# Optimization experiments

Measured on AMD Instinct MI355X. Metric: run time of the kernel, lower is better.

Reference implementation:

```python
import jax, jax.numpy as jnp
import numpy as np

WS = 4           # window_size
NUM_HEADS = 4
LN_EPS = 1e-5


def setup_inputs() -> dict:
    key = jax.random.key(0)
    ks = jax.random.split(key, 8)
    d = 256
    s = 0.02
    return {
        "feature": jax.random.normal(ks[0], (8, d, 127, 127), dtype=jnp.float32),
        "ln_w": jnp.ones((d,), jnp.float32),
        "ln_b": jnp.zeros((d,), jnp.float32),
        "in_w": jax.random.normal(ks[1], (3 * d, d), jnp.float32) * s,
        "in_b": jnp.zeros((3 * d,), jnp.float32),
        "out_w": jax.random.normal(ks[2], (d, d), jnp.float32) * s,
        "out_b": jnp.zeros((d,), jnp.float32),
        "proj_w": jax.random.normal(ks[3], (d, d), jnp.float32) * s,
        "proj_b": jnp.zeros((d,), jnp.float32),
    }


def reference(feature, ln_w, ln_b, in_w, in_b, out_w, out_b, proj_w, proj_b):
    B, C, H, W = feature.shape
    ws = WS
    pad_h = (-H) % ws
    pad_w = (-W) % ws
    x = jnp.pad(feature, ((0, 0), (0, 0), (0, pad_h), (0, pad_w)))
    Hp, Wp = H + pad_h, W + pad_w
    nh, nw = Hp // ws, Wp // ws
    # NCHW -> NHWC -> windows [B*nh*nw, ws*ws, C]
    x = x.transpose(0, 2, 3, 1)
    win = (x.reshape(B, nh, ws, nw, ws, C)
            .transpose(0, 1, 3, 2, 4, 5)
            .reshape(-1, ws * ws, C))
    # LayerNorm (ddof=0, matches torch)
    mu = win.mean(-1, keepdims=True)
    var = win.var(-1, keepdims=True)
    xn = (win - mu) / jnp.sqrt(var + LN_EPS) * ln_w + ln_b
    # fused QKV projection, then split heads
    qkv = xn @ in_w.T + in_b
    q, k, v = jnp.split(qkv, 3, axis=-1)
    hd = C // NUM_HEADS
    def heads(t):
        return t.reshape(t.shape[0], t.shape[1], NUM_HEADS, hd).transpose(0, 2, 1, 3)
    q, k, v = heads(q), heads(k), heads(v)
    scores = jnp.einsum('bhqd,bhkd->bhqk', q, k) / np.float32(np.sqrt(hd))
    a = jax.nn.softmax(scores, axis=-1)
    o = jnp.einsum('bhqk,bhkd->bhqd', a, v)
    o = o.transpose(0, 2, 1, 3).reshape(-1, ws * ws, C)
    o = o @ out_w.T + out_b
    # residual + Linear + exact GELU
    y = win + jax.nn.gelu(o @ proj_w.T + proj_b, approximate=False)
    # windows -> NHWC, crop padding, -> NCHW
    y = (y.reshape(B, nh, nw, ws, ws, C)
          .transpose(0, 1, 3, 2, 4, 5)
          .reshape(B, Hp, Wp, C))
    return y[:, :H, :W, :].transpose(0, 3, 1, 2)
```

## Files before the change

kernel.cpp:

```cpp
#include <hip/hip_runtime.h>

typedef _Float16 f16;
typedef __attribute__((ext_vector_type(4))) _Float16 half4;
typedef __attribute__((ext_vector_type(8))) _Float16 half8;
typedef __attribute__((ext_vector_type(4))) float f32x4;
typedef unsigned short u16;

#define MFMA32(a,b,c) __builtin_amdgcn_mfma_f32_16x16x32_f16(a,b,c,0,0,0)
#define MFMA16(a,b,c) __builtin_amdgcn_mfma_f32_16x16x16f16(a,b,c,0,0,0)

#define W_IN0   0
#define W_OUT0  196608
#define W_PROJ0 262144
#define X0      327680
#define QK0     33882112ull
#define VT0     100990976ull

__device__ __forceinline__ float gelu_f(float x) {
    float z = x * 0.70710678118f;
    float az = fabsf(z);
    float t = 1.f / (1.f + 0.3275911f * az);
    float e = __expf(-z * z);
    float poly = ((((1.061405429f * t - 1.453152027f) * t + 1.421413741f) * t
                   - 0.284496736f) * t + 0.254829592f) * t;
    float er = 1.f - poly * e;
    er = copysignf(er, z);
    return 0.5f * x * (1.f + er);
}

__global__ void k0_cast(const float* __restrict__ iw, const float* __restrict__ ow,
                        const float* __restrict__ pw, f16* __restrict__ W) {
    int i = blockIdx.x * 256 + threadIdx.x;
    if (i < 196608) W[W_IN0 + i] = (f16)iw[i];
    if (i < 16384) {
        const int s = i & 8191;
        const float* src = (i < 8192) ? ow : pw;
        f16* dst = W + ((i < 8192) ? W_OUT0 : W_PROJ0);
        const int g  = s & 3;
        const int r  = (s >> 2) & 31;
        const int kc = (s >> 7) & 7;
        const int ch = s >> 10;
        const int R = ch * 32 + r;
        const int c0 = kc * 32 + g * 4;
        f32x4 v0 = *(const f32x4*)(src + R * 256 + c0);
        f32x4 v1 = *(const f32x4*)(src + R * 256 + c0 + 16);
        half8 o;
#pragma unroll
        for (int j = 0; j < 4; ++j) { o[j] = (f16)v0[j]; o[j + 4] = (f16)v1[j]; }
        const int sg = g ^ ((r >> 1) & 3);
        *(half8*)(dst + ch * 8192 + kc * 1024 + r * 32 + sg * 8) = o;
    }
}

__global__ __launch_bounds__(256, 2)
void k1_pack(const float* __restrict__ feat, const float* __restrict__ lnw,
             const float* __restrict__ lnb, f16* __restrict__ X) {
    __shared__ float redS[256], redQ[256];
    const int tid = threadIdx.x;
    const int w = tid & 127, cq = tid >> 7;
    const int bid = blockIdx.x;
    const int bb = bid >> 7, h = bid & 127;
    const int c0 = cq * 128;
    const bool ok = (h < 127) && (w < 127);
    const size_t bbase = (size_t)bb * (256 * 127 * 127);
    const float* p0 = feat + bbase + (size_t)c0 * 16129 + (size_t)h * 127 + w;

    half8 ov[16];
    float s = 0.f, s2 = 0.f;
    if (ok) {
#pragma unroll
        for (int i = 0; i < 16; ++i) {
            half8 hv;
#pragma unroll
            for (int j = 0; j < 8; ++j) {
                float v = p0[(size_t)(i * 8 + j) * 16129];
                s += v; s2 += v * v; hv[j] = (f16)v;
            }
            ov[i] = hv;
        }
    } else {
#pragma unroll
        for (int i = 0; i < 16; ++i) {
            half8 hv;
#pragma unroll
            for (int j = 0; j < 8; ++j) hv[j] = (f16)0.f;
            ov[i] = hv;
        }
    }
    redS[tid] = s; redQ[tid] = s2;
    __syncthreads();
    float st = redS[w] + redS[w + 128];
    float qt = redQ[w] + redQ[w + 128];
    float mu = st * (1.f / 256.f);
    float rs = rsqrtf(qt * (1.f / 256.f) - mu * mu + 1e-5f);

    const int wi = h >> 2, hh = h & 3;
    const int jh = w >> 5, wl4 = (w >> 2) & 7, e = w & 3;
    const size_t t = ((size_t)((bb * 32 + wi) * 4 + jh)) * 128 + wl4 * 16 + hh * 4 + e;
    f16* xrow = X + t * 256 + c0;
#pragma unroll
    for (int i = 0; i < 16; ++i) {
        f32x4 lw0 = *(const f32x4*)(lnw + c0 + i * 8);
        f32x4 lw1 = *(const f32x4*)(lnw + c0 + i * 8 + 4);
        f32x4 lb0 = *(const f32x4*)(lnb + c0 + i * 8);
        f32x4 lb1 = *(const f32x4*)(lnb + c0 + i * 8 + 4);
        half8 o;
#pragma unroll
        for (int j = 0; j < 4; ++j) {
            o[j]     = (f16)(((float)ov[i][j]     - mu) * rs * lw0[j] + lb0[j]);
            o[j + 4] = (f16)(((float)ov[i][j + 4] - mu) * rs * lw1[j] + lb1[j]);
        }
        *(half8*)(xrow + i * 8) = o;
    }
}

__global__ __launch_bounds__(512, 2)
void k2_qkv(const f16* __restrict__ X, const f16* __restrict__ win,
            const float* __restrict__ inb, f16* __restrict__ QK, f16* __restrict__ VT) {
    __shared__ __align__(16) char sm[73728];
    const int tid = threadIdx.x, lane = tid & 63, wv = tid >> 6;
    const int nwg = gridDim.x;
    const int bid = (blockIdx.x & 7) * (nwg >> 3) + (blockIdx.x >> 3);
    const int mt = bid / 6, nb = bid % 6;
    const size_t Mbase = (size_t)mt * 256;
    const int n0 = nb * 128;
    const int wm = wv >> 1, wn = wv & 1;
    const int c = lane & 15, g = lane >> 4;
    const int chs = (lane & 3) ^ ((lane >> 3) & 3);

    f32x4 acc[4][4];
#pragma unroll
    for (int a = 0; a < 4; ++a)
#pragma unroll
        for (int b = 0; b < 4; ++b) acc[a][b] = f32x4{0.f, 0.f, 0.f, 0.f};

    auto stage = [&](int step, int bsel) {
        const f16* As = X + Mbase * 256 + step * 32;
        const f16* Bs = win + (size_t)n0 * 256 + step * 32;
        char* base = sm + bsel * 24576;
#pragma unroll
        for (int p = 0; p < 2; ++p) {
            int row = p * 128 + wv * 16 + (lane >> 2);
            __builtin_amdgcn_global_load_lds(
                (const __attribute__((address_space(1))) unsigned int*)(As + (size_t)row * 256 + chs * 8),
                (__attribute__((address_space(3))) unsigned int*)(base + p * 8192 + wv * 1024),
                16, 0, 0);
        }
        {
            int row = wv * 16 + (lane >> 2);
            __builtin_amdgcn_global_load_lds(
                (const __attribute__((address_space(1))) unsigned int*)(Bs + (size_t)row * 256 + chs * 8),
                (__attribute__((address_space(3))) unsigned int*)(base + 16384 + wv * 1024),
                16, 0, 0);
        }
    };
    const int rsl = (g ^ ((c >> 1) & 3)) * 16;
    auto compute = [&](int bsel) {
        char* base = sm + bsel * 24576;
        half8 a[4], b[4];
#pragma unroll
        for (int mi = 0; mi < 4; ++mi) {
            int row = wm * 64 + mi * 16 + c;
            a[mi] = *(half8*)(base + row * 64 + rsl);
        }
#pragma unroll
        for (int nt = 0; nt < 4; ++nt) {
            int row = wn * 64 + nt * 16 + c;
            b[nt] = *(half8*)(base + 16384 + row * 64 + rsl);
        }
        __builtin_amdgcn_s_setprio(1);
#pragma unroll
        for (int mi = 0; mi < 4; ++mi)
#pragma unroll
            for (int nt = 0; nt < 4; ++nt)
                acc[mi][nt] = MFMA32(a[mi], b[nt], acc[mi][nt]);
        __builtin_amdgcn_s_setprio(0);
    };

    stage(0, 0);
    stage(1, 1);
#pragma unroll
    for (int s = 0; s < 8; ++s) {
        if (s == 7) asm volatile("s_waitcnt vmcnt(0)" ::: "memory");
        else        asm volatile("s_waitcnt vmcnt(3)" ::: "memory");
        __builtin_amdgcn_s_barrier();
        if (s < 6) stage(s + 2, (s + 2) % 3);
        compute(s % 3);
    }

    const f32x4 z4 = {0.f, 0.f, 0.f, 0.f};
    half4 idf;
#pragma unroll
    for (int j = 0; j < 4; ++j) idf[j] = (f16)((g * 4 + j == c) ? 1.f : 0.f);

    if (n0 < 512) {
#pragma unroll
        for (int mi = 0; mi < 4; ++mi)
#pragma unroll
            for (int nt = 0; nt < 4; ++nt) {
                int n = n0 + wn * 64 + nt * 16 + c;
                float bias = inb[n];
                half4 h;
#pragma unroll
                for (int r = 0; r < 4; ++r) h[r] = (f16)(acc[mi][nt][r] + bias);
                f32x4 t = MFMA16(h, idf, z4);
                half4 o;
#pragma unroll
                for (int r = 0; r < 4; ++r) o[r] = (f16)t[r];
                size_t tok = Mbase + wm * 64 + mi * 16 + c;
                *(half4*)(QK + tok * 512 + (n0 + wn * 64 + nt * 16 + g * 4)) = o;
            }
    } else {
#pragma unroll
        for (int mi = 0; mi < 4; ++mi)
#pragma unroll
            for (int nt = 0; nt < 4; ++nt) {
                int n = n0 + wn * 64 + nt * 16 + c;
                float bias = inb[n];
                half4 h;
#pragma unroll
                for (int r = 0; r < 4; ++r) h[r] = (f16)(acc[mi][nt][r] + bias);
                int d = n - 512;
                size_t tokb = Mbase + wm * 64 + mi * 16;
                size_t winI = tokb >> 4;
                *(half4*)(VT + winI * 4096 + (size_t)d * 16 + g * 4) = h;
            }
    }
}

__global__ __launch_bounds__(256, 2)
void k3_attn(const f16* __restrict__ QK, const f16* __restrict__ VT,
             const f16* __restrict__ wout, const f16* __restrict__ wproj,
             const float* __restrict__ outb, const float* __restrict__ projb,
             f16* __restrict__ G) {
    __shared__ __align__(16) char sm[49152];
    const int tid = threadIdx.x, lane = tid & 63, wv = tid >> 6;
    const int c = lane & 15, g = lane >> 4;
    const size_t winA = (size_t)blockIdx.x * 8 + wv * 2;
    const size_t winB = winA + 1;
    const f16* qrowA = QK + (winA * 16 + c) * 512;
    const f16* qrowB = QK + (winB * 16 + c) * 512;
    const f32x4 z4 = {0.f, 0.f, 0.f, 0.f};

    auto stageW = [&](int it, int bsel) {
        const f16* img = (it < 8) ? (wout + it * 8192) : (wproj + (it - 8) * 8192);
#pragma unroll
        for (int q2 = 0; q2 < 4; ++q2) {
            int ia = wv * 4 + q2;
            __builtin_amdgcn_global_load_lds(
                (const __attribute__((address_space(1))) unsigned int*)(img + ia * 512 + lane * 8),
                (__attribute__((address_space(3))) unsigned int*)(sm + bsel * 16384 + ia * 1024),
                16, 0, 0);
        }
    };

    stageW(0, 0);
    stageW(1, 1);

    half8 ofpA[4][2], ofpB[4][2];
#pragma unroll
    for (int wsel = 0; wsel < 2; ++wsel) {
        const f16* qrow = wsel ? qrowB : qrowA;
        const size_t wn_ = wsel ? winB : winA;
#pragma unroll
        for (int hq = 0; hq < 4; ++hq) {
            half8 af0 = *(const half8*)(qrow + 256 + hq * 64 + g * 8);
            half8 af1 = *(const half8*)(qrow + 256 + hq * 64 + 32 + g * 8);
            half8 bq0 = *(const half8*)(qrow + hq * 64 + g * 8);
            half8 bq1 = *(const half8*)(qrow + hq * 64 + 32 + g * 8);
            f32x4 sacc = MFMA32(af0, bq0, z4);
            sacc = MFMA32(af1, bq1, sacc);
            float s0 = sacc[0] * 0.125f, s1 = sacc[1] * 0.125f;
            float s2 = sacc[2] * 0.125f, s3 = sacc[3] * 0.125f;
            float mx = fmaxf(fmaxf(s0, s1), fmaxf(s2, s3));
            mx = fmaxf(mx, __shfl_xor(mx, 16));
            mx = fmaxf(mx, __shfl_xor(mx, 32));
            float p0 = __expf(s0 - mx), p1 = __expf(s1 - mx);
            float p2 = __expf(s2 - mx), p3 = __expf(s3 - mx);
            float sum = p0 + p1 + p2 + p3;
            sum += __shfl_xor(sum, 16);
            sum += __shfl_xor(sum, 32);
            float inv = 1.f / sum;
            half4 pf;
            pf[0] = (f16)(p0 * inv); pf[1] = (f16)(p1 * inv);
            pf[2] = (f16)(p2 * inv); pf[3] = (f16)(p3 * inv);
#pragma unroll
            for (int nt = 0; nt < 4; ++nt) {
                half4 vf = *(const half4*)(VT + wn_ * 4096 + (size_t)(hq * 64 + nt * 16 + c) * 16 + g * 4);
                f32x4 o = MFMA16(vf, pf, z4);
#pragma unroll
                for (int r = 0; r < 4; ++r) {
                    if (wsel) ofpB[hq][nt >> 1][(nt & 1) * 4 + r] = (f16)o[r];
                    else      ofpA[hq][nt >> 1][(nt & 1) * 4 + r] = (f16)o[r];
                }
            }
        }
    }

    const int rsl = (g ^ ((c >> 1) & 3)) * 16;
    half8 obpA[8], obpB[8];

#pragma unroll
    for (int it = 0; it < 16; ++it) {
        if (it == 15)     asm volatile("s_waitcnt vmcnt(4)" ::: "memory");
        else if (it >= 9) asm volatile("s_waitcnt vmcnt(8)" ::: "memory");
        else              asm volatile("s_waitcnt vmcnt(4)" ::: "memory");
        __builtin_amdgcn_s_barrier();
        if (it < 14) stageW(it + 2, (it + 2) % 3);
        char* base = sm + (it % 3) * 16384;
        f32x4 aA0 = z4, aA1 = z4, aB0 = z4, aB1 = z4;
        __builtin_amdgcn_s_setprio(1);
        if (it < 8) {
#pragma unroll
            for (int kc = 0; kc < 8; ++kc) {
                half8 w0 = *(half8*)(base + kc * 2048 + c * 64 + rsl);
                aA0 = MFMA32(w0, ofpA[kc >> 1][kc & 1], aA0);
                aB0 = MFMA32(w0, ofpB[kc >> 1][kc & 1], aB0);
                half8 w1 = *(half8*)(base + kc * 2048 + 1024 + c * 64 + rsl);
                aA1 = MFMA32(w1, ofpA[kc >> 1][kc & 1], aA1);
                aB1 = MFMA32(w1, ofpB[kc >> 1][kc & 1], aB1);
            }
        } else {
#pragma unroll
            for (int kc = 0; kc < 8; ++kc) {
                half8 w0 = *(half8*)(base + kc * 2048 + c * 64 + rsl);
                aA0 = MFMA32(w0, obpA[kc], aA0);
                aB0 = MFMA32(w0, obpB[kc], aB0);
                half8 w1 = *(half8*)(base + kc * 2048 + 1024 + c * 64 + rsl);
                aA1 = MFMA32(w1, obpA[kc], aA1);
                aB1 = MFMA32(w1, obpB[kc], aB1);
            }
        }
        __builtin_amdgcn_s_setprio(0);
        if (it < 8) {
            const int ch = it;
            f32x4 b0 = *(const f32x4*)(outb + ch * 32 + g * 4);
            f32x4 b1 = *(const f32x4*)(outb + ch * 32 + 16 + g * 4);
#pragma unroll
            for (int r = 0; r < 4; ++r) {
                obpA[ch][r]     = (f16)(aA0[r] + b0[r]);
                obpA[ch][4 + r] = (f16)(aA1[r] + b1[r]);
                obpB[ch][r]     = (f16)(aB0[r] + b0[r]);
                obpB[ch][4 + r] = (f16)(aB1[r] + b1[r]);
            }
        } else {
            const int pc = it - 8;
            f32x4 b0 = *(const f32x4*)(projb + pc * 32 + g * 4);
            f32x4 b1 = *(const f32x4*)(projb + pc * 32 + 16 + g * 4);
            half4 hA0, hA1, hB0, hB1;
#pragma unroll
            for (int r = 0; r < 4; ++r) {
                hA0[r] = (f16)gelu_f(aA0[r] + b0[r]);
                hA1[r] = (f16)gelu_f(aA1[r] + b1[r]);
                hB0[r] = (f16)gelu_f(aB0[r] + b0[r]);
                hB1[r] = (f16)gelu_f(aB1[r] + b1[r]);
            }
            f16* growA = G + (winA * 16 + c) * 256 + pc * 32;
            *(half4*)(growA + g * 4) = hA0;
            *(half4*)(growA + 16 + g * 4) = hA1;
            f16* growB = G + (winB * 16 + c) * 256 + pc * 32;
            *(half4*)(growB + g * 4) = hB0;
            *(half4*)(growB + 16 + g * 4) = hB1;
        }
    }
}

__global__ __launch_bounds__(256, 8)
void k4_out(const f16* __restrict__ G, const float* __restrict__ feat, float* __restrict__ outp) {
    const int tid = threadIdx.x;
    const int bid = blockIdx.x;
    const int bb = bid / 127, h = bid % 127;
    const int w = tid & 127;
    const int cq = tid >> 7;
    const bool wok = (w < 127);
    const size_t bbase = (size_t)bb * (256 * 127 * 127);
    const int wi = h >> 2, hh = h & 3;
    const int jh = w >> 5, wl4 = (w >> 2) & 7, e = w & 3;
    const size_t t = ((size_t)((bb * 32 + wi) * 4 + jh)) * 128 + wl4 * 16 + hh * 4 + e;
    const f16* gp = G + t * 256;
    const float* fp = feat + bbase + (size_t)h * 127 + w;
    float* op = outp + bbase + (size_t)h * 127 + w;
#pragma unroll 4
    for (int ci = 0; ci < 32; ++ci) {
        const int ch = ci * 8 + cq * 4;
        if (wok) {
            half4 g4 = *(const half4*)(gp + ch);
#pragma unroll
            for (int j = 0; j < 4; ++j) {
                size_t off = (size_t)(ch + j) * 16129;
                op[off] = fp[off] + (float)g4[j];
            }
        }
    }
}

extern "C" void kernel_launch(void* const* d_in, const int* in_sizes, int n_in,
                              void* d_out, int out_size, void* d_ws, size_t ws_size,
                              hipStream_t stream) {
    const float* feat   = (const float*)d_in[0];
    const float* ln_w   = (const float*)d_in[1];
    const float* ln_b   = (const float*)d_in[2];
    const float* in_w   = (const float*)d_in[3];
    const float* in_b   = (const float*)d_in[4];
    const float* out_w  = (const float*)d_in[5];
    const float* out_b  = (const float*)d_in[6];
    const float* proj_w = (const float*)d_in[7];
    const float* proj_b = (const float*)d_in[8];

    f16* W  = (f16*)d_ws;
    f16* Xb  = W + X0;
    f16* QKb = W + QK0;
    f16* VTb = W + VT0;
    f16* Gb  = Xb;

    k0_cast<<<768, 256, 0, stream>>>(in_w, out_w, proj_w, W);
    k1_pack<<<1024, 256, 0, stream>>>(feat, ln_w, ln_b, Xb);
    k2_qkv<<<3072, 512, 0, stream>>>(Xb, W + W_IN0, in_b, QKb, VTb);
    k3_attn<<<1024, 256, 0, stream>>>(QKb, VTb, W + W_OUT0, W + W_PROJ0, out_b, proj_b, Gb);
    k4_out<<<1016, 256, 0, stream>>>(Gb, feat, (float*)d_out);
}
```

Measured before the change: 333.4 us.

## Split fused attention+GEMM kernel into separate attention and projection kernels

The attention computation (QK^T, softmax, PV) is moved out of the fused kernel into its own kernel, which writes per-window outputs to a workspace buffer. A second kernel reloads those outputs and runs the out/proj GEMMs with the LDS-staged weight pipeline. The aim is to let the attention part run at higher parallelism and to shorten the GEMM kernel's prologue, so weight staging is not stalled behind the attention math. The cost is an extra global round trip of the attention output and one more launch. Buffer reuse also changes: the output goes into Xb and G goes into the QK region.

```diff
diff --git a/kernel.cpp b/kernel.cpp
--- a/kernel.cpp
+++ b/kernel.cpp
@@ -229,17 +229,63 @@
 }
 
 __global__ __launch_bounds__(256, 2)
-void k3_attn(const f16* __restrict__ QK, const f16* __restrict__ VT,
-             const f16* __restrict__ wout, const f16* __restrict__ wproj,
-             const float* __restrict__ outb, const float* __restrict__ projb,
-             f16* __restrict__ G) {
+void k3a_attn(const f16* __restrict__ QK, const f16* __restrict__ VT,
+              f16* __restrict__ O) {
+    const int tid = threadIdx.x, lane = tid & 63, wv = tid >> 6;
+    const int c = lane & 15, g = lane >> 4;
+    const size_t win = (size_t)blockIdx.x * 4 + wv;
+    const f16* qrow = QK + (win * 16 + c) * 512;
+    const f32x4 z4 = {0.f, 0.f, 0.f, 0.f};
+
+    half8 ofp[4][2];
+#pragma unroll
+    for (int hq = 0; hq < 4; ++hq) {
+        half8 af0 = *(const half8*)(qrow + 256 + hq * 64 + g * 8);
+        half8 af1 = *(const half8*)(qrow + 256 + hq * 64 + 32 + g * 8);
+        half8 bq0 = *(const half8*)(qrow + hq * 64 + g * 8);
+        half8 bq1 = *(const half8*)(qrow + hq * 64 + 32 + g * 8);
+        f32x4 sacc = MFMA32(af0, bq0, z4);
+        sacc = MFMA32(af1, bq1, sacc);
+        float s0 = sacc[0] * 0.125f, s1 = sacc[1] * 0.125f;
+        float s2 = sacc[2] * 0.125f, s3 = sacc[3] * 0.125f;
+        float mx = fmaxf(fmaxf(s0, s1), fmaxf(s2, s3));
+        mx = fmaxf(mx, __shfl_xor(mx, 16));
+        mx = fmaxf(mx, __shfl_xor(mx, 32));
+        float p0 = __expf(s0 - mx), p1 = __expf(s1 - mx);
+        float p2 = __expf(s2 - mx), p3 = __expf(s3 - mx);
+        float sum = p0 + p1 + p2 + p3;
+        sum += __shfl_xor(sum, 16);
+        sum += __shfl_xor(sum, 32);
+        float inv = 1.f / sum;
+        half4 pf;
+        pf[0] = (f16)(p0 * inv); pf[1] = (f16)(p1 * inv);
+        pf[2] = (f16)(p2 * inv); pf[3] = (f16)(p3 * inv);
+#pragma unroll
+        for (int nt = 0; nt < 4; ++nt) {
+            half4 vf = *(const half4*)(VT + win * 4096 + (size_t)(hq * 64 + nt * 16 + c) * 16 + g * 4);
+            f32x4 o = MFMA16(vf, pf, z4);
+#pragma unroll
+            for (int r = 0; r < 4; ++r) ofp[hq][nt >> 1][(nt & 1) * 4 + r] = (f16)o[r];
+        }
+    }
+    f16* obase = O + win * 4096 + c * 32 + g * 8;
+#pragma unroll
+    for (int hq = 0; hq < 4; ++hq)
+#pragma unroll
+        for (int p = 0; p < 2; ++p)
+            *(half8*)(obase + hq * 1024 + p * 512) = ofp[hq][p];
+}
+
+__global__ __launch_bounds__(256, 2)
+void k3b_gemm(const f16* __restrict__ O,
+              const f16* __restrict__ wout, const f16* __restrict__ wproj,
+              const float* __restrict__ outb, const float* __restrict__ projb,
+              f16* __restrict__ G) {
     __shared__ __align__(16) char sm[49152];
     const int tid = threadIdx.x, lane = tid & 63, wv = tid >> 6;
     const int c = lane & 15, g = lane >> 4;
     const size_t winA = (size_t)blockIdx.x * 8 + wv * 2;
     const size_t winB = winA + 1;
-    const f16* qrowA = QK + (winA * 16 + c) * 512;
-    const f16* qrowB = QK + (winB * 16 + c) * 512;
     const f32x4 z4 = {0.f, 0.f, 0.f, 0.f};
 
     auto stageW = [&](int it, int bsel) {
@@ -254,48 +300,19 @@
         }
     };
 
+    half8 ofpA[4][2], ofpB[4][2];
+    const f16* oA = O + winA * 4096 + c * 32 + g * 8;
+    const f16* oB = O + winB * 4096 + c * 32 + g * 8;
+#pragma unroll
+    for (int hq = 0; hq < 4; ++hq)
+#pragma unroll
+        for (int p = 0; p < 2; ++p) {
+            ofpA[hq][p] = *(const half8*)(oA + hq * 1024 + p * 512);
+            ofpB[hq][p] = *(const half8*)(oB + hq * 1024 + p * 512);
+        }
+
     stageW(0, 0);
     stageW(1, 1);
-
-    half8 ofpA[4][2], ofpB[4][2];
-#pragma unroll
-    for (int wsel = 0; wsel < 2; ++wsel) {
-        const f16* qrow = wsel ? qrowB : qrowA;
-        const size_t wn_ = wsel ? winB : winA;
-#pragma unroll
-        for (int hq = 0; hq < 4; ++hq) {
-            half8 af0 = *(const half8*)(qrow + 256 + hq * 64 + g * 8);
-            half8 af1 = *(const half8*)(qrow + 256 + hq * 64 + 32 + g * 8);
-            half8 bq0 = *(const half8*)(qrow + hq * 64 + g * 8);
-            half8 bq1 = *(const half8*)(qrow + hq * 64 + 32 + g * 8);
-            f32x4 sacc = MFMA32(af0, bq0, z4);
-            sacc = MFMA32(af1, bq1, sacc);
-            float s0 = sacc[0] * 0.125f, s1 = sacc[1] * 0.125f;
-            float s2 = sacc[2] * 0.125f, s3 = sacc[3] * 0.125f;
-            float mx = fmaxf(fmaxf(s0, s1), fmaxf(s2, s3));
-            mx = fmaxf(mx, __shfl_xor(mx, 16));
-            mx = fmaxf(mx, __shfl_xor(mx, 32));
-            float p0 = __expf(s0 - mx), p1 = __expf(s1 - mx);
-            float p2 = __expf(s2 - mx), p3 = __expf(s3 - mx);
-            float sum = p0 + p1 + p2 + p3;
-            sum += __shfl_xor(sum, 16);
-            sum += __shfl_xor(sum, 32);
-            float inv = 1.f / sum;
-            half4 pf;
-            pf[0] = (f16)(p0 * inv); pf[1] = (f16)(p1 * inv);
-            pf[2] = (f16)(p2 * inv); pf[3] = (f16)(p3 * inv);
-#pragma unroll
-            for (int nt = 0; nt < 4; ++nt) {
-                half4 vf = *(const half4*)(VT + wn_ * 4096 + (size_t)(hq * 64 + nt * 16 + c) * 16 + g * 4);
-                f32x4 o = MFMA16(vf, pf, z4);
-#pragma unroll
-                for (int r = 0; r < 4; ++r) {
-                    if (wsel) ofpB[hq][nt >> 1][(nt & 1) * 4 + r] = (f16)o[r];
-                    else      ofpA[hq][nt >> 1][(nt & 1) * 4 + r] = (f16)o[r];
-                }
-            }
-        }
-    }
 
     const int rsl = (g ^ ((c >> 1) & 3)) * 16;
     half8 obpA[8], obpB[8];
@@ -407,15 +424,15 @@
     const float* proj_w = (const float*)d_in[7];
     const float* proj_b = (const float*)d_in[8];
 
-    f16* W  = (f16*)d_ws;
+    f16* W   = (f16*)d_ws;
     f16* Xb  = W + X0;
     f16* QKb = W + QK0;
     f16* VTb = W + VT0;
-    f16* Gb  = Xb;
 
     k0_cast<<<768, 256, 0, stream>>>(in_w, out_w, proj_w, W);
     k1_pack<<<1024, 256, 0, stream>>>(feat, ln_w, ln_b, Xb);
     k2_qkv<<<3072, 512, 0, stream>>>(Xb, W + W_IN0, in_b, QKb, VTb);
-    k3_attn<<<1024, 256, 0, stream>>>(QKb, VTb, W + W_OUT0, W + W_PROJ0, out_b, proj_b, Gb);
-    k4_out<<<1016, 256, 0, stream>>>(Gb, feat, (float*)d_out);
-}
+    k3a_attn<<<2048, 256, 0, stream>>>(QKb, VTb, Xb);
+    k3b_gemm<<<1024, 256, 0, stream>>>(Xb, W + W_OUT0, W + W_PROJ0, out_b, proj_b, QKb);
+    k4_out<<<1016, 256, 0, stream>>>(QKb, feat, (float*)d_out);
+}
```

Result: slower. 369.1 us (+10.7%).
